# Kernel optimization log

Hardware: AMD Instinct MI355X
Metric: run time of the kernel (lower is better)

## Reference

```python
import jax, jax.numpy as jnp
import numpy as np

# Standard FP4 E2M1 lookup table (nvfp4-style): sign bit in nibble MSB.
FP4_LUT = jnp.array([0.0, 0.5, 1.0, 1.5, 2.0, 3.0, 4.0, 6.0,
                     -0.0, -0.5, -1.0, -1.5, -2.0, -3.0, -4.0, -6.0],
                    dtype=jnp.float32)


def dequant_fp4(packed_i32, scales, group_size):
    """packed_i32: [K/8, N] int32 (8 fp4 nibbles per word, low nibble first);
    scales: [K/group_size, N]. Returns dense fp32 weight [K, N]."""
    w = jax.lax.bitcast_convert_type(packed_i32, jnp.uint32)  # [K/8, N]
    # Unpack nibbles along the reduction axis: nibble i -> row 8*r + i.
    nib = jnp.stack([(w >> jnp.uint32(4 * i)) & jnp.uint32(0xF) for i in range(8)],
                    axis=1)                                    # [K/8, 8, N]
    K = nib.shape[0] * 8
    nib = nib.reshape(K, w.shape[1])                           # [K, N]
    vals = FP4_LUT[nib]                                        # [K, N]
    s = jnp.repeat(scales, group_size, axis=0)                 # [K, N]
    return vals * s


def setup_inputs() -> dict:
    key = jax.random.key(0)
    k1, k2, k3, k4, k5, k6 = jax.random.split(key, 6)
    tokens, H, I, G = 4096, 2048, 5632, 128
    return {
        "hidden": jax.random.normal(k1, (tokens, H), dtype=jnp.float32),
        "moe_output": jax.random.normal(k2, (tokens, H), dtype=jnp.float32),
        "gate_up_weights": jax.random.randint(k3, (H // 8, 2 * I), 0, 2147483647, dtype=jnp.int32),
        "gate_up_scales": jax.random.uniform(k4, (H // G, 2 * I), dtype=jnp.float32, minval=0.01, maxval=0.1),
        "down_weights": jax.random.randint(k5, (I // 8, H), 0, 2147483647, dtype=jnp.int32),
        "down_scales": jax.random.uniform(k6, (I // G, H), dtype=jnp.float32, minval=0.01, maxval=0.1),
        "group_size": G,
    }


def reference(hidden, moe_output, gate_up_weights, gate_up_scales,
              down_weights, down_scales, group_size):
    # Shared-expert SwiGLU FFN with FP4 group-quantized weights, fused residual add.
    W_gu = dequant_fp4(gate_up_weights, gate_up_scales, group_size)  # [H, 2I]
    gu = hidden @ W_gu                                               # [T, 2I]
    I = gu.shape[1] // 2
    gate, up = gu[:, :I], gu[:, I:]
    act = jax.nn.silu(gate) * up                                     # [T, I]
    W_d = dequant_fp4(down_weights, down_scales, group_size)         # [I, H]
    return moe_output + act @ W_d                                    # [T, H]
```

## Files before the change

kernel.cpp:

```cpp
#include <hip/hip_runtime.h>
#include <hip/hip_fp16.h>
#include <stdint.h>

#define TOKENS 4096
#define HDIM   2048
#define IDIM   5632
#define BM 128
#define BN 128
#define BK 64

typedef _Float16 f16x8 __attribute__((ext_vector_type(8)));
typedef float    f32x4 __attribute__((ext_vector_type(4)));

__device__ __forceinline__ uint32_t dec2(uint32_t z, uint32_t s2u) {
    uint32_t sgn = (z << 12) & 0x80008000u;
    uint32_t h   = ((z << 9) & 0x0E000E00u) | sgn;
    __half2 hv = __builtin_bit_cast(__half2, h);
    __half2 sv = __builtin_bit_cast(__half2, s2u);
    __half2 r  = __hmul2(hv, sv);
    return __builtin_bit_cast(uint32_t, r);
}

__device__ __forceinline__ uint32_t packh(float lo, float hi) {
    __half2 h2 = __halves2half2(__float2half(lo), __float2half(hi));
    return __builtin_bit_cast(uint32_t, h2);
}

__global__ __launch_bounds__(256) void convert_hidden(
    const float* __restrict__ src, __half* __restrict__ dst)
{
    int idx = blockIdx.x * 256 + threadIdx.x;
    const float4* s = (const float4*)src + (size_t)idx * 2;
    float4 a = s[0], b = s[1];
    int4 v;
    v.x = (int)packh(a.x, b.x);
    v.y = (int)packh(a.y, b.y);
    v.z = (int)packh(a.z, b.z);
    v.w = (int)packh(a.w, b.w);
    *((int4*)dst + idx) = v;
}

__global__ __launch_bounds__(256, 2) void gemm1_silu(
    const __half* __restrict__ A, const uint32_t* __restrict__ W,
    const float* __restrict__ S, __half* __restrict__ act)
{
    __shared__ __half Alds[BM * BK];
    __shared__ __half Blds[2][BN * BK];
    const int tid  = threadIdx.x;
    const int lane = tid & 63;
    const int wid  = tid >> 6;
    const int wm = wid >> 1, wn = wid & 1;
    const int m0 = blockIdx.y * BM;
    const int c0 = blockIdx.x * BN;

    f32x4 accg[4][4], accu[4][4];
    #pragma unroll
    for (int i = 0; i < 4; ++i)
        #pragma unroll
        for (int j = 0; j < 4; ++j) {
            accg[i][j] = f32x4{0.f, 0.f, 0.f, 0.f};
            accu[i][j] = f32x4{0.f, 0.f, 0.f, 0.f};
        }

    const int c = tid & 127;
    const int rbase = (tid >> 7) * 4;

    for (int kt = 0; kt < HDIM / BK; ++kt) {
        const int k0 = kt * BK;
        #pragma unroll
        for (int i = 0; i < 4; ++i) {
            int u = tid + i * 256;
            int row = u >> 3, kb = u & 7;
            int4 v = *(const int4*)(A + (size_t)(m0 + row) * HDIM + k0 + kb * 8);
            *(int4*)((char*)Alds + row * 128 + ((kb ^ (row & 7)) << 4)) = v;
        }
        const int g = k0 >> 7;
        #pragma unroll
        for (int p = 0; p < 2; ++p) {
            const int ncol = (p ? IDIM : 0) + c0 + c;
            float sc = S[(size_t)g * (2 * IDIM) + ncol] * 16384.0f;
            uint16_t hs = __builtin_bit_cast(uint16_t, __float2half(sc));
            uint32_t s2u = (uint32_t)hs * 0x00010001u;
            #pragma unroll
            for (int i = 0; i < 4; ++i) {
                int rl = rbase + i;
                uint32_t w = W[(size_t)(kt * 8 + rl) * (2 * IDIM) + ncol];
                int4 d;
                d.x = (int)dec2( w        & 0x000F000Fu, s2u);
                d.y = (int)dec2((w >> 4)  & 0x000F000Fu, s2u);
                d.z = (int)dec2((w >> 8)  & 0x000F000Fu, s2u);
                d.w = (int)dec2((w >> 12) & 0x000F000Fu, s2u);
                *(int4*)((char*)&Blds[p][0] + c * 128 + ((rl ^ (c & 7)) << 4)) = d;
            }
        }
        __syncthreads();
        #pragma unroll
        for (int ks = 0; ks < 2; ++ks) {
            f16x8 af[4], bg[4], bu[4];
            const int kb = ks * 4 + (lane >> 4);
            #pragma unroll
            for (int mi = 0; mi < 4; ++mi) {
                int m = wm * 64 + mi * 16 + (lane & 15);
                af[mi] = *(const f16x8*)((const char*)Alds + m * 128 + ((kb ^ (m & 7)) << 4));
            }
            #pragma unroll
            for (int ni = 0; ni < 4; ++ni) {
                int n = wn * 64 + ni * 16 + (lane & 15);
                bg[ni] = *(const f16x8*)((const char*)&Blds[0][0] + n * 128 + ((kb ^ (n & 7)) << 4));
                bu[ni] = *(const f16x8*)((const char*)&Blds[1][0] + n * 128 + ((kb ^ (n & 7)) << 4));
            }
            #pragma unroll
            for (int mi = 0; mi < 4; ++mi)
                #pragma unroll
                for (int ni = 0; ni < 4; ++ni) {
                    accg[mi][ni] = __builtin_amdgcn_mfma_f32_16x16x32_f16(af[mi], bg[ni], accg[mi][ni], 0, 0, 0);
                    accu[mi][ni] = __builtin_amdgcn_mfma_f32_16x16x32_f16(af[mi], bu[ni], accu[mi][ni], 0, 0, 0);
                }
        }
        __syncthreads();
    }
    #pragma unroll
    for (int mi = 0; mi < 4; ++mi) {
        #pragma unroll
        for (int ni = 0; ni < 4; ++ni) {
            int nlog = c0 + wn * 64 + ni * 16 + (lane & 15);
            int ncol = (nlog & ~7) | (((nlog & 3) << 1) | ((nlog >> 2) & 1));
            #pragma unroll
            for (int r = 0; r < 4; ++r) {
                int m = m0 + wm * 64 + mi * 16 + (lane >> 4) * 4 + r;
                float gv = accg[mi][ni][r];
                float uv = accu[mi][ni][r];
                float sig = 1.0f / (1.0f + __expf(-gv));
                act[(size_t)m * IDIM + ncol] = __float2half(gv * sig * uv);
            }
        }
    }
}

__global__ __launch_bounds__(256, 2) void gemm2_add(
    const __half* __restrict__ A, const uint32_t* __restrict__ W,
    const float* __restrict__ S, const float* __restrict__ moe,
    float* __restrict__ out)
{
    __shared__ __half Alds[BM * BK];
    __shared__ __half Blds[BN * BK];
    const int tid  = threadIdx.x;
    const int lane = tid & 63;
    const int wid  = tid >> 6;
    const int wm = wid >> 1, wn = wid & 1;
    const int m0 = blockIdx.y * BM;
    const int n0 = blockIdx.x * BN;

    f32x4 acc[4][4];
    #pragma unroll
    for (int i = 0; i < 4; ++i)
        #pragma unroll
        for (int j = 0; j < 4; ++j) acc[i][j] = f32x4{0.f, 0.f, 0.f, 0.f};

    const int c = tid & 127;
    const int rbase = (tid >> 7) * 4;

    for (int kt = 0; kt < IDIM / BK; ++kt) {
        const int k0 = kt * BK;
        #pragma unroll
        for (int i = 0; i < 4; ++i) {
            int u = tid + i * 256;
            int row = u >> 3, kb = u & 7;
            int4 v = *(const int4*)(A + (size_t)(m0 + row) * IDIM + k0 + kb * 8);
            *(int4*)((char*)Alds + row * 128 + ((kb ^ (row & 7)) << 4)) = v;
        }
        {
            const int g = k0 >> 7;
            const int ncol = n0 + c;
            float sc = S[(size_t)g * HDIM + ncol] * 16384.0f;
            uint16_t hs = __builtin_bit_cast(uint16_t, __float2half(sc));
            uint32_t s2u = (uint32_t)hs * 0x00010001u;
            #pragma unroll
            for (int i = 0; i < 4; ++i) {
                int rl = rbase + i;
                uint32_t w = W[(size_t)(kt * 8 + rl) * HDIM + ncol];
                int4 d;
                d.x = (int)dec2( w        & 0x000F000Fu, s2u);
                d.y = (int)dec2((w >> 4)  & 0x000F000Fu, s2u);
                d.z = (int)dec2((w >> 8)  & 0x000F000Fu, s2u);
                d.w = (int)dec2((w >> 12) & 0x000F000Fu, s2u);
                *(int4*)((char*)Blds + c * 128 + ((rl ^ (c & 7)) << 4)) = d;
            }
        }
        __syncthreads();
        #pragma unroll
        for (int ks = 0; ks < 2; ++ks) {
            f16x8 af[4], bf[4];
            const int kb = ks * 4 + (lane >> 4);
            #pragma unroll
            for (int mi = 0; mi < 4; ++mi) {
                int m = wm * 64 + mi * 16 + (lane & 15);
                af[mi] = *(const f16x8*)((const char*)Alds + m * 128 + ((kb ^ (m & 7)) << 4));
            }
            #pragma unroll
            for (int ni = 0; ni < 4; ++ni) {
                int n = wn * 64 + ni * 16 + (lane & 15);
                bf[ni] = *(const f16x8*)((const char*)Blds + n * 128 + ((kb ^ (n & 7)) << 4));
            }
            #pragma unroll
            for (int mi = 0; mi < 4; ++mi)
                #pragma unroll
                for (int ni = 0; ni < 4; ++ni)
                    acc[mi][ni] = __builtin_amdgcn_mfma_f32_16x16x32_f16(af[mi], bf[ni], acc[mi][ni], 0, 0, 0);
        }
        __syncthreads();
    }
    #pragma unroll
    for (int mi = 0; mi < 4; ++mi) {
        #pragma unroll
        for (int ni = 0; ni < 4; ++ni) {
            int n = n0 + wn * 64 + ni * 16 + (lane & 15);
            #pragma unroll
            for (int r = 0; r < 4; ++r) {
                int m = m0 + wm * 64 + mi * 16 + (lane >> 4) * 4 + r;
                out[(size_t)m * HDIM + n] = moe[(size_t)m * HDIM + n] + acc[mi][ni][r];
            }
        }
    }
}

extern "C" void kernel_launch(void* const* d_in, const int* in_sizes, int n_in,
                              void* d_out, int out_size, void* d_ws, size_t ws_size,
                              hipStream_t stream) {
    const float*    hidden = (const float*)d_in[0];
    const float*    moe    = (const float*)d_in[1];
    const uint32_t* wgu    = (const uint32_t*)d_in[2];
    const float*    sgu    = (const float*)d_in[3];
    const uint32_t* wd     = (const uint32_t*)d_in[4];
    const float*    sd     = (const float*)d_in[5];
    float* out = (float*)d_out;

    __half* hidden_f16 = (__half*)d_ws;
    __half* act        = (__half*)((char*)d_ws + (size_t)TOKENS * HDIM * 2);

    convert_hidden<<<dim3(TOKENS * HDIM / 8 / 256), dim3(256), 0, stream>>>(hidden, hidden_f16);
    gemm1_silu<<<dim3(IDIM / BN, TOKENS / BM), dim3(256), 0, stream>>>(hidden_f16, wgu, sgu, act);
    gemm2_add<<<dim3(HDIM / BN, TOKENS / BM), dim3(256), 0, stream>>>(act, wd, sd, moe, out);
}
```

Before: 334.4 us.

## Predequantize gate/up weights and use pipelined direct-to-LDS GEMM1 kernel

Adds a separate kernel that dequantizes the FP4 gate/up weights once per call into a pre-swizzled fp16 transposed buffer in workspace. A new 512-thread GEMM1 with 256x128 tiles then streams A and B through triple-buffered LDS using global_load_lds, interleaving loads with MFMA phases and applying block swizzling for L2 locality. Gate and up columns are paired inside each tile, and the SiLU output is written with a permuted column order. The goal is to take the per-tile dequant work out of the GEMM inner loop and hide load latency, at the price of extra workspace and an extra pass over memory for the dequant. It only runs when the workspace is large enough, so whether it is active depends on ws_size.

```diff
diff --git a/kernel.cpp b/kernel.cpp
--- a/kernel.cpp
+++ b/kernel.cpp
@@ -20,16 +20,35 @@
     __half2 r  = __hmul2(hv, sv);
     return __builtin_bit_cast(uint32_t, r);
 }
-
+__device__ __forceinline__ int4 dec8(uint32_t w, uint32_t s2u) {
+    int4 d;
+    d.x = (int)dec2( w        & 0x000F000Fu, s2u);
+    d.y = (int)dec2((w >> 4)  & 0x000F000Fu, s2u);
+    d.z = (int)dec2((w >> 8)  & 0x000F000Fu, s2u);
+    d.w = (int)dec2((w >> 12) & 0x000F000Fu, s2u);
+    return d;
+}
+__device__ __forceinline__ uint32_t scale_s2u(float sc) {
+    uint16_t hs = __builtin_bit_cast(uint16_t, __float2half(sc * 16384.0f));
+    return (uint32_t)hs * 0x00010001u;
+}
 __device__ __forceinline__ uint32_t packh(float lo, float hi) {
     __half2 h2 = __halves2half2(__float2half(lo), __float2half(hi));
     return __builtin_bit_cast(uint32_t, h2);
 }
-
+__device__ __forceinline__ void gl_lds16(const void* g, void* l) {
+    __builtin_amdgcn_global_load_lds(
+        (const __attribute__((address_space(1))) uint32_t*)g,
+        (__attribute__((address_space(3))) uint32_t*)l, 16, 0, 0);
+}
+
+template<bool PRESWZ>
 __global__ __launch_bounds__(256) void convert_hidden(
     const float* __restrict__ src, __half* __restrict__ dst)
 {
     int idx = blockIdx.x * 256 + threadIdx.x;
+    int m  = idx >> 8;
+    int kb = idx & 255;
     const float4* s = (const float4*)src + (size_t)idx * 2;
     float4 a = s[0], b = s[1];
     int4 v;
@@ -37,7 +56,138 @@
     v.y = (int)packh(a.y, b.y);
     v.z = (int)packh(a.z, b.z);
     v.w = (int)packh(a.w, b.w);
-    *((int4*)dst + idx) = v;
+    int slot = PRESWZ ? ((kb & 7) ^ (m & 7)) : (kb & 7);
+    *(int4*)(dst + (size_t)m * HDIM + (kb & ~7) * 8 + slot * 8) = v;
+}
+
+__global__ __launch_bounds__(256) void dequant_wgu(
+    const uint32_t* __restrict__ W, const float* __restrict__ S,
+    __half* __restrict__ Bt)
+{
+    int np = blockIdx.x * 256 + threadIdx.x;
+    int within = np & 15;
+    int pair = np >> 5;
+    int sel  = (np >> 4) & 1;
+    int sc = pair * 16 + within + (sel ? IDIM : 0);
+    int x = np & 7;
+    #pragma unroll
+    for (int q = 0; q < 4; ++q) {
+        int kt = blockIdx.y * 4 + q;
+        uint32_t s2u = scale_s2u(S[(size_t)(kt >> 1) * (2 * IDIM) + sc]);
+        #pragma unroll
+        for (int g = 0; g < 8; ++g) {
+            uint32_t w = W[(size_t)(kt * 8 + g) * (2 * IDIM) + sc];
+            int4 d = dec8(w, s2u);
+            *(int4*)(Bt + (size_t)np * HDIM + kt * 64 + ((g ^ x) << 3)) = d;
+        }
+    }
+}
+
+#define G1_BM 256
+#define G1_BN 128
+#define G1_BK 64
+#define G1_NT (HDIM / G1_BK)
+
+__global__ __launch_bounds__(512, 1) void gemm1_8ph(
+    const __half* __restrict__ A, const __half* __restrict__ Bt,
+    __half* __restrict__ act)
+{
+    __shared__ __half Al[3][G1_BM * G1_BK];
+    __shared__ __half Bl[3][G1_BN * G1_BK];
+    const int tid  = threadIdx.x;
+    const int lane = tid & 63;
+    const int wid  = tid >> 6;
+    const int wm   = wid >> 2;
+    const int wn   = wid & 3;
+
+    int bid = blockIdx.x;
+    int swz = (bid & 7) * (1408 / 8) + (bid >> 3);
+    int by = swz / 88, bx = swz % 88;
+    const int m0 = by * G1_BM;
+    const int n0 = bx * G1_BN;
+
+    int ia0 = tid, ia1 = 512 + tid, ia2 = 1024 + tid, ia3 = 1536 + tid;
+    const __half* preA0 = A + (size_t)(m0 + (ia0 >> 3)) * HDIM + (ia0 & 7) * 8;
+    const __half* preA1 = A + (size_t)(m0 + (ia1 >> 3)) * HDIM + (ia1 & 7) * 8;
+    const __half* preA2 = A + (size_t)(m0 + (ia2 >> 3)) * HDIM + (ia2 & 7) * 8;
+    const __half* preA3 = A + (size_t)(m0 + (ia3 >> 3)) * HDIM + (ia3 & 7) * 8;
+    const __half* preB0 = Bt + (size_t)(n0 + (ia0 >> 3)) * HDIM + (ia0 & 7) * 8;
+    const __half* preB1 = Bt + (size_t)(n0 + (ia1 >> 3)) * HDIM + (ia1 & 7) * 8;
+
+    auto stg3a = [&](int buf, int kt) {
+        gl_lds16(preA0 + (size_t)kt * G1_BK, &Al[buf][(0    + wid * 64) * 8]);
+        gl_lds16(preA1 + (size_t)kt * G1_BK, &Al[buf][(512  + wid * 64) * 8]);
+        gl_lds16(preB0 + (size_t)kt * G1_BK, &Bl[buf][(0    + wid * 64) * 8]);
+    };
+    auto stg3b = [&](int buf, int kt) {
+        gl_lds16(preA2 + (size_t)kt * G1_BK, &Al[buf][(1024 + wid * 64) * 8]);
+        gl_lds16(preA3 + (size_t)kt * G1_BK, &Al[buf][(1536 + wid * 64) * 8]);
+        gl_lds16(preB1 + (size_t)kt * G1_BK, &Bl[buf][(512  + wid * 64) * 8]);
+    };
+
+    f32x4 acc[8][2];
+    #pragma unroll
+    for (int i = 0; i < 8; ++i) {
+        acc[i][0] = f32x4{0.f, 0.f, 0.f, 0.f};
+        acc[i][1] = f32x4{0.f, 0.f, 0.f, 0.f};
+    }
+
+    auto phase = [&](const __half* Ac, const __half* Bc, int ks) {
+        f16x8 af[8], bf[2];
+        int kb = ks * 4 + (lane >> 4);
+        #pragma unroll
+        for (int mi = 0; mi < 8; ++mi) {
+            int r = wm * 128 + mi * 16 + (lane & 15);
+            af[mi] = *(const f16x8*)&Ac[r * 64 + ((kb ^ (r & 7)) << 3)];
+        }
+        #pragma unroll
+        for (int ni = 0; ni < 2; ++ni) {
+            int r = wn * 32 + ni * 16 + (lane & 15);
+            bf[ni] = *(const f16x8*)&Bc[r * 64 + ((kb ^ (r & 7)) << 3)];
+        }
+        __builtin_amdgcn_s_setprio(1);
+        #pragma unroll
+        for (int mi = 0; mi < 8; ++mi)
+            #pragma unroll
+            for (int ni = 0; ni < 2; ++ni)
+                acc[mi][ni] = __builtin_amdgcn_mfma_f32_16x16x32_f16(af[mi], bf[ni], acc[mi][ni], 0, 0, 0);
+        __builtin_amdgcn_s_setprio(0);
+    };
+
+    stg3a(0, 0); stg3b(0, 0);
+    stg3a(1, 1); stg3b(1, 1);
+    asm volatile("s_waitcnt vmcnt(6)" ::: "memory");
+    __builtin_amdgcn_s_barrier();
+
+    for (int kt = 0; kt < G1_NT; ++kt) {
+        int cur = kt % 3;
+        int nxt = cur + 2; if (nxt >= 3) nxt -= 3;
+        bool st = (kt + 2) < G1_NT;
+        if (st) stg3a(nxt, kt + 2);
+        phase(&Al[cur][0], &Bl[cur][0], 0);
+        __builtin_amdgcn_s_barrier();
+        if (st) stg3b(nxt, kt + 2);
+        phase(&Al[cur][0], &Bl[cur][0], 1);
+        asm volatile("s_waitcnt lgkmcnt(0)" ::: "memory");
+        if (kt < G1_NT - 2) asm volatile("s_waitcnt vmcnt(6)" ::: "memory");
+        else                asm volatile("s_waitcnt vmcnt(0)" ::: "memory");
+        __builtin_amdgcn_s_barrier();
+    }
+
+    const int j0 = (bx * 4 + wn) * 16;
+    int ja = j0 + (lane & 15);
+    int colstore = (ja & ~7) | (((ja & 3) << 1) | ((ja >> 2) & 1));
+    #pragma unroll
+    for (int mi = 0; mi < 8; ++mi) {
+        #pragma unroll
+        for (int r = 0; r < 4; ++r) {
+            int m = m0 + wm * 128 + mi * 16 + (lane >> 4) * 4 + r;
+            float gv = acc[mi][0][r];
+            float uv = acc[mi][1][r];
+            float sig = 1.0f / (1.0f + __expf(-gv));
+            act[(size_t)m * IDIM + colstore] = __float2half(gv * sig * uv);
+        }
+    }
 }
 
 __global__ __launch_bounds__(256, 2) void gemm1_silu(
@@ -78,18 +228,12 @@
         #pragma unroll
         for (int p = 0; p < 2; ++p) {
             const int ncol = (p ? IDIM : 0) + c0 + c;
-            float sc = S[(size_t)g * (2 * IDIM) + ncol] * 16384.0f;
-            uint16_t hs = __builtin_bit_cast(uint16_t, __float2half(sc));
-            uint32_t s2u = (uint32_t)hs * 0x00010001u;
+            uint32_t s2u = scale_s2u(S[(size_t)g * (2 * IDIM) + ncol]);
             #pragma unroll
             for (int i = 0; i < 4; ++i) {
                 int rl = rbase + i;
                 uint32_t w = W[(size_t)(kt * 8 + rl) * (2 * IDIM) + ncol];
-                int4 d;
-                d.x = (int)dec2( w        & 0x000F000Fu, s2u);
-                d.y = (int)dec2((w >> 4)  & 0x000F000Fu, s2u);
-                d.z = (int)dec2((w >> 8)  & 0x000F000Fu, s2u);
-                d.w = (int)dec2((w >> 12) & 0x000F000Fu, s2u);
+                int4 d = dec8(w, s2u);
                 *(int4*)((char*)&Blds[p][0] + c * 128 + ((rl ^ (c & 7)) << 4)) = d;
             }
         }
@@ -172,18 +316,12 @@
         {
             const int g = k0 >> 7;
             const int ncol = n0 + c;
-            float sc = S[(size_t)g * HDIM + ncol] * 16384.0f;
-            uint16_t hs = __builtin_bit_cast(uint16_t, __float2half(sc));
-            uint32_t s2u = (uint32_t)hs * 0x00010001u;
+            uint32_t s2u = scale_s2u(S[(size_t)g * HDIM + ncol]);
             #pragma unroll
             for (int i = 0; i < 4; ++i) {
                 int rl = rbase + i;
                 uint32_t w = W[(size_t)(kt * 8 + rl) * HDIM + ncol];
-                int4 d;
-                d.x = (int)dec2( w        & 0x000F000Fu, s2u);
-                d.y = (int)dec2((w >> 4)  & 0x000F000Fu, s2u);
-                d.z = (int)dec2((w >> 8)  & 0x000F000Fu, s2u);
-                d.w = (int)dec2((w >> 12) & 0x000F000Fu, s2u);
+                int4 d = dec8(w, s2u);
                 *(int4*)((char*)Blds + c * 128 + ((rl ^ (c & 7)) << 4)) = d;
             }
         }
@@ -237,8 +375,18 @@
 
     __half* hidden_f16 = (__half*)d_ws;
     __half* act        = (__half*)((char*)d_ws + (size_t)TOKENS * HDIM * 2);
-
-    convert_hidden<<<dim3(TOKENS * HDIM / 8 / 256), dim3(256), 0, stream>>>(hidden, hidden_f16);
-    gemm1_silu<<<dim3(IDIM / BN, TOKENS / BM), dim3(256), 0, stream>>>(hidden_f16, wgu, sgu, act);
+    size_t need = (size_t)TOKENS * HDIM * 2 + (size_t)TOKENS * IDIM * 2
+                + (size_t)HDIM * (2 * IDIM) * 2;
+
+    if (ws_size >= need) {
+        __half* wgu16 = (__half*)((char*)d_ws + (size_t)TOKENS * HDIM * 2
+                                              + (size_t)TOKENS * IDIM * 2);
+        convert_hidden<true><<<dim3(TOKENS * HDIM / 8 / 256), dim3(256), 0, stream>>>(hidden, hidden_f16);
+        dequant_wgu<<<dim3(2 * IDIM / 256, 8), dim3(256), 0, stream>>>(wgu, sgu, wgu16);
+        gemm1_8ph<<<dim3(1408), dim3(512), 0, stream>>>(hidden_f16, wgu16, act);
+    } else {
+        convert_hidden<false><<<dim3(TOKENS * HDIM / 8 / 256), dim3(256), 0, stream>>>(hidden, hidden_f16);
+        gemm1_silu<<<dim3(IDIM / BN, TOKENS / BM), dim3(256), 0, stream>>>(hidden_f16, wgu, sgu, act);
+    }
     gemm2_add<<<dim3(HDIM / BN, TOKENS / BM), dim3(256), 0, stream>>>(act, wd, sd, moe, out);
 }
```

Result: slower. 466.7 us (+39.6%).

## Pre-dequantize gate/up weights to fp16 and stream them via global_load_lds

Applied to the files above, without the earlier changes.

Adds a separate kernel that dequantizes the FP4 gate/up weights once per call into an fp16 buffer in the workspace. The buffer uses a K-tiled, interleaved gate/up column layout. A new gemm1 kernel then loads both A and B tiles straight into LDS with global_load_lds, with no per-tile decode work, and handles SiLU in the epilogue through a column permutation. This removes the decode ALU work repeated in every M-block, at the cost of writing and re-reading a 46MB fp16 weight buffer. The new path runs only when the workspace is large enough; otherwise it falls back to the old kernel.

```diff
diff --git a/kernel.cpp b/kernel.cpp
--- a/kernel.cpp
+++ b/kernel.cpp
@@ -8,6 +8,9 @@
 #define BM 128
 #define BN 128
 #define BK 64
+
+#define G1_NP  11264
+#define G1_KSB (G1_NP * 64)
 
 typedef _Float16 f16x8 __attribute__((ext_vector_type(8)));
 typedef float    f32x4 __attribute__((ext_vector_type(4)));
@@ -20,10 +23,26 @@
     __half2 r  = __hmul2(hv, sv);
     return __builtin_bit_cast(uint32_t, r);
 }
-
+__device__ __forceinline__ int4 dec8(uint32_t w, uint32_t s2u) {
+    int4 d;
+    d.x = (int)dec2( w        & 0x000F000Fu, s2u);
+    d.y = (int)dec2((w >> 4)  & 0x000F000Fu, s2u);
+    d.z = (int)dec2((w >> 8)  & 0x000F000Fu, s2u);
+    d.w = (int)dec2((w >> 12) & 0x000F000Fu, s2u);
+    return d;
+}
+__device__ __forceinline__ uint32_t scale_s2u(float sc) {
+    uint16_t hs = __builtin_bit_cast(uint16_t, __float2half(sc * 16384.0f));
+    return (uint32_t)hs * 0x00010001u;
+}
 __device__ __forceinline__ uint32_t packh(float lo, float hi) {
     __half2 h2 = __halves2half2(__float2half(lo), __float2half(hi));
     return __builtin_bit_cast(uint32_t, h2);
+}
+__device__ __forceinline__ void gl_lds16(const void* g, void* l) {
+    __builtin_amdgcn_global_load_lds(
+        (const __attribute__((address_space(1))) uint32_t*)g,
+        (__attribute__((address_space(3))) uint32_t*)l, 16, 0, 0);
 }
 
 __global__ __launch_bounds__(256) void convert_hidden(
@@ -40,6 +59,100 @@
     *((int4*)dst + idx) = v;
 }
 
+__global__ __launch_bounds__(256) void dequant_wgu(
+    const uint32_t* __restrict__ W, const float* __restrict__ S,
+    __half* __restrict__ Bt)
+{
+    int kt = blockIdx.y;
+    int np = blockIdx.x * 32 + (threadIdx.x >> 3);
+    int j  = threadIdx.x & 7;
+    int within = np & 15;
+    int pair   = np >> 5;
+    int sel    = (np >> 4) & 1;
+    int sc = pair * 16 + within + (sel ? IDIM : 0);
+    uint32_t s2u = scale_s2u(S[(size_t)(kt >> 1) * (2 * IDIM) + sc]);
+    uint32_t w   = W[(size_t)(kt * 8 + j) * (2 * IDIM) + sc];
+    int4 d = dec8(w, s2u);
+    *(int4*)(Bt + (size_t)kt * G1_KSB + (size_t)np * 64 + j * 8) = d;
+}
+
+__global__ __launch_bounds__(256, 4) void gemm1_s(
+    const __half* __restrict__ A, const __half* __restrict__ Bt,
+    __half* __restrict__ act)
+{
+    __shared__ __half Alds[BM * 64];
+    __shared__ __half Blds[BN * 64];
+    const int tid  = threadIdx.x;
+    const int lane = tid & 63;
+    const int wid  = tid >> 6;
+    const int wm = wid >> 1, wn = wid & 1;
+    const int m0 = blockIdx.y * BM;
+    const int n0 = blockIdx.x * BN;
+
+    f32x4 acc[4][4];
+    #pragma unroll
+    for (int i = 0; i < 4; ++i)
+        #pragma unroll
+        for (int j = 0; j < 4; ++j) acc[i][j] = f32x4{0.f, 0.f, 0.f, 0.f};
+
+    const __half* srcA[4];
+    const __half* srcB[4];
+    #pragma unroll
+    for (int i = 0; i < 4; ++i) {
+        int u = i * 256 + tid, row = u >> 3, s = u & 7, sl = s ^ (row & 7);
+        srcA[i] = A  + (size_t)(m0 + row) * HDIM + sl * 8;
+        srcB[i] = Bt + (size_t)(n0 + row) * 64 + sl * 8;
+    }
+
+    for (int kt = 0; kt < HDIM / 64; ++kt) {
+        #pragma unroll
+        for (int i = 0; i < 4; ++i) {
+            int u = i * 256 + tid;
+            gl_lds16(srcA[i] + (size_t)kt * 64,      (char*)Alds + u * 16);
+            gl_lds16(srcB[i] + (size_t)kt * G1_KSB,  (char*)Blds + u * 16);
+        }
+        __syncthreads();
+        #pragma unroll
+        for (int ks = 0; ks < 2; ++ks) {
+            f16x8 af[4], bf[4];
+            const int kb = ks * 4 + (lane >> 4);
+            #pragma unroll
+            for (int mi = 0; mi < 4; ++mi) {
+                int r = wm * 64 + mi * 16 + (lane & 15);
+                af[mi] = *(const f16x8*)&Alds[r * 64 + ((kb ^ (r & 7)) << 3)];
+            }
+            #pragma unroll
+            for (int ni = 0; ni < 4; ++ni) {
+                int r = wn * 64 + ni * 16 + (lane & 15);
+                bf[ni] = *(const f16x8*)&Blds[r * 64 + ((kb ^ (r & 7)) << 3)];
+            }
+            #pragma unroll
+            for (int mi = 0; mi < 4; ++mi)
+                #pragma unroll
+                for (int ni = 0; ni < 4; ++ni)
+                    acc[mi][ni] = __builtin_amdgcn_mfma_f32_16x16x32_f16(af[mi], bf[ni], acc[mi][ni], 0, 0, 0);
+        }
+        __syncthreads();
+    }
+
+    #pragma unroll
+    for (int mi = 0; mi < 4; ++mi) {
+        #pragma unroll
+        for (int q = 0; q < 2; ++q) {
+            int gc = ((n0 + wn * 64 + q * 32) >> 5) * 16 + (lane & 15);
+            int colstore = (gc & ~7) | (((gc & 3) << 1) | ((gc >> 2) & 1));
+            #pragma unroll
+            for (int r = 0; r < 4; ++r) {
+                int m = m0 + wm * 64 + mi * 16 + (lane >> 4) * 4 + r;
+                float gv = acc[mi][2 * q][r];
+                float uv = acc[mi][2 * q + 1][r];
+                float sig = 1.0f / (1.0f + __expf(-gv));
+                act[(size_t)m * IDIM + colstore] = __float2half(gv * sig * uv);
+            }
+        }
+    }
+}
+
 __global__ __launch_bounds__(256, 2) void gemm1_silu(
     const __half* __restrict__ A, const uint32_t* __restrict__ W,
     const float* __restrict__ S, __half* __restrict__ act)
@@ -78,18 +191,12 @@
         #pragma unroll
         for (int p = 0; p < 2; ++p) {
             const int ncol = (p ? IDIM : 0) + c0 + c;
-            float sc = S[(size_t)g * (2 * IDIM) + ncol] * 16384.0f;
-            uint16_t hs = __builtin_bit_cast(uint16_t, __float2half(sc));
-            uint32_t s2u = (uint32_t)hs * 0x00010001u;
+            uint32_t s2u = scale_s2u(S[(size_t)g * (2 * IDIM) + ncol]);
             #pragma unroll
             for (int i = 0; i < 4; ++i) {
                 int rl = rbase + i;
                 uint32_t w = W[(size_t)(kt * 8 + rl) * (2 * IDIM) + ncol];
-                int4 d;
-                d.x = (int)dec2( w        & 0x000F000Fu, s2u);
-                d.y = (int)dec2((w >> 4)  & 0x000F000Fu, s2u);
-                d.z = (int)dec2((w >> 8)  & 0x000F000Fu, s2u);
-                d.w = (int)dec2((w >> 12) & 0x000F000Fu, s2u);
+                int4 d = dec8(w, s2u);
                 *(int4*)((char*)&Blds[p][0] + c * 128 + ((rl ^ (c & 7)) << 4)) = d;
             }
         }
@@ -172,18 +279,12 @@
         {
             const int g = k0 >> 7;
             const int ncol = n0 + c;
-            float sc = S[(size_t)g * HDIM + ncol] * 16384.0f;
-            uint16_t hs = __builtin_bit_cast(uint16_t, __float2half(sc));
-            uint32_t s2u = (uint32_t)hs * 0x00010001u;
+            uint32_t s2u = scale_s2u(S[(size_t)g * HDIM + ncol]);
             #pragma unroll
             for (int i = 0; i < 4; ++i) {
                 int rl = rbase + i;
                 uint32_t w = W[(size_t)(kt * 8 + rl) * HDIM + ncol];
-                int4 d;
-                d.x = (int)dec2( w        & 0x000F000Fu, s2u);
-                d.y = (int)dec2((w >> 4)  & 0x000F000Fu, s2u);
-                d.z = (int)dec2((w >> 8)  & 0x000F000Fu, s2u);
-                d.w = (int)dec2((w >> 12) & 0x000F000Fu, s2u);
+                int4 d = dec8(w, s2u);
                 *(int4*)((char*)Blds + c * 128 + ((rl ^ (c & 7)) << 4)) = d;
             }
         }
@@ -237,8 +338,17 @@
 
     __half* hidden_f16 = (__half*)d_ws;
     __half* act        = (__half*)((char*)d_ws + (size_t)TOKENS * HDIM * 2);
+    size_t need = (size_t)TOKENS * HDIM * 2 + (size_t)TOKENS * IDIM * 2
+                + (size_t)HDIM * (2 * IDIM) * 2;
 
     convert_hidden<<<dim3(TOKENS * HDIM / 8 / 256), dim3(256), 0, stream>>>(hidden, hidden_f16);
-    gemm1_silu<<<dim3(IDIM / BN, TOKENS / BM), dim3(256), 0, stream>>>(hidden_f16, wgu, sgu, act);
+    if (ws_size >= need) {
+        __half* wgu16 = (__half*)((char*)d_ws + (size_t)TOKENS * HDIM * 2
+                                              + (size_t)TOKENS * IDIM * 2);
+        dequant_wgu<<<dim3(G1_NP / 32, 32), dim3(256), 0, stream>>>(wgu, sgu, wgu16);
+        gemm1_s<<<dim3(IDIM * 2 / BN, TOKENS / BM), dim3(256), 0, stream>>>(hidden_f16, wgu16, act);
+    } else {
+        gemm1_silu<<<dim3(IDIM / BN, TOKENS / BM), dim3(256), 0, stream>>>(hidden_f16, wgu, sgu, act);
+    }
     gemm2_add<<<dim3(HDIM / BN, TOKENS / BM), dim3(256), 0, stream>>>(act, wd, sd, moe, out);
 }
```

Result: no change. 328.8 us (-1.7%).
